# Performance work log

Hardware: AMD Instinct MI355X
Metric: run time of the kernel (lower is better)

## Reference

```python
import jax, jax.numpy as jnp
import numpy as np

# (in_ch, out_ch) per conv layer per SA stage (use_xyz adds +3 to first in-ch)
DIMS = {1: [(3, 64), (64, 64), (64, 128)],
        2: [(131, 128), (128, 128), (128, 256)],
        3: [(259, 256), (256, 512), (512, 1024)]}
B, N = 32, 4096


def setup_inputs() -> dict:
    key = jax.random.key(0)
    key, k = jax.random.split(key)
    inp = {"pointcloud": jax.random.uniform(k, (B, N, 3), jnp.float32)}
    for s in (1, 2, 3):
        for l, (ci, co) in enumerate(DIMS[s]):
            key, k1, k2, k3 = jax.random.split(key, 4)
            inp[f"w{s}{l}"] = jax.random.normal(k1, (ci, co), jnp.float32) * (1.0 / np.sqrt(ci))
            # eval-mode BatchNorm folded to per-channel scale g and bias b
            inp[f"g{s}{l}"] = 1.0 + 0.1 * jax.random.normal(k2, (co,), jnp.float32)
            inp[f"b{s}{l}"] = 0.1 * jax.random.normal(k3, (co,), jnp.float32)
    return inp


def fps(xyz, npoint):
    """Farthest point sampling. xyz: (B,N,3) -> idx (B,npoint) int32. First index is 0."""
    n = xyz.shape[1]
    def one(pts):
        def body(carry, _):
            dist, last = carry
            d = jnp.sum((pts - pts[last]) ** 2, axis=-1)
            dist = jnp.minimum(dist, d)
            nxt = jnp.argmax(dist).astype(jnp.int32)
            return (dist, nxt), nxt
        init = (jnp.full((n,), 1e10, pts.dtype), jnp.int32(0))
        _, idxs = jax.lax.scan(body, init, None, length=npoint - 1)
        return jnp.concatenate([jnp.zeros((1,), jnp.int32), idxs])
    return jax.vmap(one)(xyz)


def ball_query(xyz, centers, radius, nsample):
    """xyz (B,N,3), centers (B,S,3) -> idx (B,S,nsample): first nsample in-ball point
    indices, deficits padded with the first found index (matches CUDA ball_query)."""
    n = xyz.shape[1]
    d2 = jnp.sum((centers[:, :, None, :] - xyz[:, None, :, :]) ** 2, axis=-1)  # (B,S,N)
    keyv = jnp.where(d2 < radius * radius, jnp.arange(n)[None, None, :], n)
    sk = jnp.sort(keyv, axis=-1)[..., :nsample]  # ascending valid indices, pad = n
    first = sk[..., :1]
    idx = jnp.where(sk == n, first, sk)
    return jnp.clip(idx, 0, n - 1)


def gather(pts, idx):
    """pts (B,N,C), idx (B,...) -> (B,...,C)"""
    return jax.vmap(lambda p, i: p[i])(pts, idx)


def shared_mlp(x, params):
    """x (..., Cin); each layer: 1x1 conv (matmul) + folded-BN affine + ReLU."""
    for w, g, b in params:
        x = jax.nn.relu(jnp.einsum('...c,cd->...d', x, w) * g + b)
    return x


def sa_module(xyz, feat, npoint, radius, nsample, params):
    ctr_idx = fps(xyz, npoint)
    new_xyz = gather(xyz, ctr_idx)                        # (B,S,3)
    idx = ball_query(xyz, new_xyz, radius, nsample)       # (B,S,K)
    g_xyz = gather(xyz, idx) - new_xyz[:, :, None, :]     # (B,S,K,3) centered
    grouped = g_xyz if feat is None else jnp.concatenate([g_xyz, gather(feat, idx)], axis=-1)
    h = shared_mlp(grouped, params)                       # (B,S,K,Cout)
    return new_xyz, jnp.max(h, axis=2)                    # max-pool over neighbors


def reference(pointcloud, w10, g10, b10, w11, g11, b11, w12, g12, b12,
              w20, g20, b20, w21, g21, b21, w22, g22, b22,
              w30, g30, b30, w31, g31, b31, w32, g32, b32):
    p1 = [(w10, g10, b10), (w11, g11, b11), (w12, g12, b12)]
    p2 = [(w20, g20, b20), (w21, g21, b21), (w22, g22, b22)]
    p3 = [(w30, g30, b30), (w31, g31, b31), (w32, g32, b32)]
    xyz = pointcloud[..., :3]
    xyz, feat = sa_module(xyz, None, 512, 0.2, 64, p1)
    xyz, feat = sa_module(xyz, feat, 128, 0.4, 64, p2)
    # group-all SA: one group containing all points, xyz NOT centered
    grouped = jnp.concatenate([xyz, feat], axis=-1)[:, None]  # (B,1,S,259)
    h = shared_mlp(grouped, p3)                                # (B,1,S,1024)
    return jnp.max(h, axis=2)[:, 0]                            # (B,1024)
```

## Files before the change

### kernel.cpp

```cpp
#include <hip/hip_runtime.h>
#include <math.h>

#define NTH 256

using short8 = __attribute__((ext_vector_type(8))) short;
using f32x4  = __attribute__((ext_vector_type(4))) float;

__device__ __forceinline__ unsigned short f2bf(float x) {
    unsigned u = __float_as_uint(x);
    u += 0x7fff + ((u >> 16) & 1);
    return (unsigned short)(u >> 16);
}
__device__ __forceinline__ float bf2f(unsigned short h) {
    return __uint_as_float(((unsigned)h) << 16);
}

template<int CTRL>
__device__ __forceinline__ unsigned long long dppmax(unsigned long long k) {
    unsigned lo = (unsigned)k, hi = (unsigned)(k >> 32);
    unsigned plo = (unsigned)__builtin_amdgcn_update_dpp(0, (int)lo, CTRL, 0xF, 0xF, true);
    unsigned phi = (unsigned)__builtin_amdgcn_update_dpp(0, (int)hi, CTRL, 0xF, 0xF, true);
    unsigned long long p = ((unsigned long long)phi << 32) | plo;
    return p > k ? p : k;
}

template<int N, int NPOINT, int NTHR>
__device__ __forceinline__ void fps_body(
    const float* __restrict__ xyz, float* __restrict__ out_xyz, int b,
    float* __restrict__ pts , float* __restrict__ ctr ,
    unsigned long long* __restrict__ wkey )
{
    constexpr int PT = N / NTHR;
    constexpr int NW = NTHR / 64;
    const int tid  = threadIdx.x;
    const int lane = tid & 63;
    const int w    = tid >> 6;
    const float* src = xyz + (size_t)b * N * 3;

    for (int e = tid; e < N * 3; e += NTHR) pts[e] = src[e];

    float px[PT], py[PT], pz[PT], dist[PT];
    unsigned klo[PT];
#pragma unroll
    for (int j = 0; j < PT; ++j) {
        int i = j * NTHR + tid;
        px[j] = src[i * 3 + 0]; py[j] = src[i * 3 + 1]; pz[j] = src[i * 3 + 2];
        dist[j] = 1e10f;
        klo[j] = ~(unsigned)i;
    }
    if (tid == 0) { ctr[0] = src[0]; ctr[1] = src[1]; ctr[2] = src[2]; }
    __syncthreads();

    int last = 0;
    for (int it = 1; it < NPOINT; ++it) {
        const float lx = pts[last * 3 + 0];
        const float ly = pts[last * 3 + 1];
        const float lz = pts[last * 3 + 2];
        unsigned long long best = 0ull;
#pragma unroll
        for (int j = 0; j < PT; ++j) {
            float dx = px[j] - lx, dy = py[j] - ly, dz = pz[j] - lz;
            float d = __fadd_rn(__fadd_rn(__fmul_rn(dx, dx), __fmul_rn(dy, dy)),
                                __fmul_rn(dz, dz));
            float nd = fminf(dist[j], d);
            dist[j] = nd;
            unsigned long long key =
                ((unsigned long long)__float_as_uint(nd) << 32) | (unsigned long long)klo[j];
            best = (key > best) ? key : best;
        }
        best = dppmax<0xB1>(best);
        best = dppmax<0x4E>(best);
        best = dppmax<0x141>(best);
        best = dppmax<0x140>(best);
        best = dppmax<0x142>(best);
        best = dppmax<0x143>(best);
        const int p = (it & 1) * NW;
        if (lane == 63) wkey[p + w] = best;
        __syncthreads();
        unsigned long long K0[NW];
#pragma unroll
        for (int v = 0; v < NW; ++v) K0[v] = wkey[p + v];
#pragma unroll
        for (int st = NW / 2; st > 0; st >>= 1)
#pragma unroll
            for (int v = 0; v < st; ++v) K0[v] = (K0[v + st] > K0[v]) ? K0[v + st] : K0[v];
        last = (int)(~(unsigned)K0[0]);
        if (tid == 0) {
            ctr[it * 3 + 0] = pts[last * 3 + 0];
            ctr[it * 3 + 1] = pts[last * 3 + 1];
            ctr[it * 3 + 2] = pts[last * 3 + 2];
        }
    }
    __syncthreads();
    float* dst = out_xyz + (size_t)b * NPOINT * 3;
    for (int e = tid; e < NPOINT * 3; e += NTHR) dst[e] = ctr[e];
}

#define PREP_TOT 813056
__device__ __forceinline__ void prep_body(
    int gid, int stride,
    const float* __restrict__ w0, const float* __restrict__ w1, const float* __restrict__ w2,
    const float* __restrict__ w3, const float* __restrict__ w4, const float* __restrict__ w5,
    const float* __restrict__ w6, const float* __restrict__ w7, const float* __restrict__ w8,
    unsigned short* __restrict__ outw)
{
    const int K_[9]    = {3, 64, 64, 131, 128, 128, 259, 256, 512};
    const int N_[9]    = {64, 64, 128, 128, 128, 256, 256, 512, 1024};
    const int E_[9]    = {2048, 4096, 8192, 20480, 16384, 32768, 73728, 131072, 524288};
    const int base_[9] = {0, 4096, 12288, 28672, 69632, 102400, 167936, 315392, 577536};
    const int PCF_[9]  = {0, 0, 0, 128, 0, 0, 256, 0, 0};
    const float* W_[9] = {w0, w1, w2, w3, w4, w5, w6, w7, w8};
    for (; gid < PREP_TOT; gid += stride) {
        int i = 0, t = gid;
        while (t >= E_[i]) { t -= E_[i]; ++i; }
        const int Nn = N_[i];
        const int k8 = t / (Nn * 8);
        const int rem = t - k8 * Nn * 8;
        const int col = rem >> 3, j = rem & 7;
        const int k = k8 * 8 + j;
        float v = 0.f;
        if (k < K_[i]) {
            int ks = k;
            const int pcf = PCF_[i];
            if (pcf > 0) ks = (k < pcf) ? (k + 3) : (k - pcf);
            v = W_[i][(size_t)ks * Nn + col];
        }
        unsigned short hi = f2bf(v);
        unsigned short lo = f2bf(v - bf2f(hi));
        outw[base_[i] + t] = hi;
        outw[base_[i] + E_[i] + t] = lo;
    }
}

template<int N1, int NP1>
__global__ __launch_bounds__(NTH) void fps1_prep(
    const float* __restrict__ pc, float* __restrict__ nxyz1,
    const float* __restrict__ w0, const float* __restrict__ w1, const float* __restrict__ w2,
    const float* __restrict__ w3, const float* __restrict__ w4, const float* __restrict__ w5,
    const float* __restrict__ w6, const float* __restrict__ w7, const float* __restrict__ w8,
    unsigned short* __restrict__ outw, int nfps)
{
    __shared__ float pts[N1 * 3];
    __shared__ float ctr[NP1 * 3];
    __shared__ unsigned long long fwk[2 * (NTH / 64)];
    if ((int)blockIdx.x < nfps) {
        fps_body<N1, NP1, NTH>(pc, nxyz1, blockIdx.x, pts, ctr, fwk);
    } else {
        prep_body((blockIdx.x - nfps) * NTH + threadIdx.x,
                  (gridDim.x - nfps) * NTH,
                  w0, w1, w2, w3, w4, w5, w6, w7, w8, outw);
    }
}

__global__ __launch_bounds__(NTH) void ball_query_kernel(
    const float* __restrict__ xyz, const float* __restrict__ centers,
    int* __restrict__ out, int BS, int N, int S, float r2)
{
    const int wid = blockIdx.x * (NTH / 64) + (threadIdx.x >> 6);
    if (wid >= BS) return;
    const int lane = threadIdx.x & 63;
    const int b = wid / S;
    const float cx = centers[(size_t)wid * 3 + 0];
    const float cy = centers[(size_t)wid * 3 + 1];
    const float cz = centers[(size_t)wid * 3 + 2];
    const float* px = xyz + (size_t)b * N * 3;
    int count = 0, first = -1;
    for (int base = 0; base < N && count < 64; base += 64) {
        int i = base + lane;
        float dx = px[i * 3 + 0] - cx, dy = px[i * 3 + 1] - cy, dz = px[i * 3 + 2] - cz;
        float d2 = __fadd_rn(__fadd_rn(__fmul_rn(dx, dx), __fmul_rn(dy, dy)),
                             __fmul_rn(dz, dz));
        bool inb = d2 < r2;
        unsigned long long m = __ballot(inb);
        if (first < 0 && m) first = base + (__ffsll(m) - 1);
        if (inb) {
            int pos = count + (int)__popcll(m & ((1ull << lane) - 1ull));
            if (pos < 64) out[(size_t)wid * 64 + pos] = i;
        }
        count += (int)__popcll(m);
    }
    int cnt = count > 64 ? 64 : count;
    if (first < 0) first = N - 1;
    if (lane >= cnt) out[(size_t)wid * 64 + lane] = first;
}

template<int K, int NSUB, int NOFF, int NFULL, int RTILES, int SX, int SY, bool FINAL>
__device__ __forceinline__ void mfma_layer(
    const unsigned short* __restrict__ whi, const unsigned short* __restrict__ wlo,
    const float* __restrict__ gm, const float* __restrict__ bt,
    const unsigned short* __restrict__ Xhi, const unsigned short* __restrict__ Xlo,
    unsigned short* __restrict__ Yhi, unsigned short* __restrict__ Ylo,
    float* outp, int tid)
{
    constexpr int KP  = (K + 31) & ~31;
    constexpr int KC  = KP / 32;
    constexpr int NTW = NSUB / 64;
    static_assert(NSUB % 64 == 0, "col split");
    const int w = tid >> 6, lane = tid & 63;
    const int lr = lane & 15, lg = lane >> 4;
    const int colbase = NOFF + w * (NSUB / 4);

    f32x4 acc[RTILES][NTW];
#pragma unroll
    for (int m = 0; m < RTILES; ++m)
#pragma unroll
        for (int t = 0; t < NTW; ++t) acc[m][t] = f32x4{0.f, 0.f, 0.f, 0.f};

    const unsigned short* xh0 = Xhi + lr * SX + lg * 8;
    const unsigned short* xl0 = Xlo + lr * SX + lg * 8;

    for (int kc = 0; kc < KC; ++kc) {
        const size_t krow = (size_t)(kc * 4 + lg) * NFULL * 8;
        short8 bh[NTW], bl[NTW];
#pragma unroll
        for (int t = 0; t < NTW; ++t) {
            const int col = colbase + t * 16 + lr;
            bh[t] = *reinterpret_cast<const short8*>(whi + krow + (size_t)col * 8);
            bl[t] = *reinterpret_cast<const short8*>(wlo + krow + (size_t)col * 8);
        }
#pragma unroll
        for (int m = 0; m < RTILES; ++m) {
            short8 ah = *reinterpret_cast<const short8*>(xh0 + m * 16 * SX + kc * 32);
            short8 al = *reinterpret_cast<const short8*>(xl0 + m * 16 * SX + kc * 32);
#pragma unroll
            for (int t = 0; t < NTW; ++t) {
                acc[m][t] = __builtin_amdgcn_mfma_f32_16x16x32_bf16(ah, bh[t], acc[m][t], 0, 0, 0);
                acc[m][t] = __builtin_amdgcn_mfma_f32_16x16x32_bf16(ah, bl[t], acc[m][t], 0, 0, 0);
                acc[m][t] = __builtin_amdgcn_mfma_f32_16x16x32_bf16(al, bh[t], acc[m][t], 0, 0, 0);
            }
        }
    }
#pragma unroll
    for (int t = 0; t < NTW; ++t) {
        const int col = colbase + t * 16 + lr;
        const float gv = gm[col], bv = bt[col];
        if constexpr (FINAL) {
            float mx = 0.f;
#pragma unroll
            for (int m = 0; m < RTILES; ++m)
#pragma unroll
                for (int r = 0; r < 4; ++r)
                    mx = fmaxf(mx, fmaxf(fmaf(acc[m][t][r], gv, bv), 0.f));
            mx = fmaxf(mx, __shfl_xor(mx, 16));
            mx = fmaxf(mx, __shfl_xor(mx, 32));
            if (lg == 0)
                atomicMax(reinterpret_cast<int*>(outp) + col, __float_as_int(mx));
        } else {
#pragma unroll
            for (int m = 0; m < RTILES; ++m)
#pragma unroll
                for (int r = 0; r < 4; ++r) {
                    float v = fmaxf(fmaf(acc[m][t][r], gv, bv), 0.f);
                    unsigned short hi = f2bf(v);
                    unsigned short lo = f2bf(v - bf2f(hi));
                    const int row = m * 16 + lg * 4 + r;
                    Yhi[row * SY + col] = hi;
                    Ylo[row * SY + col] = lo;
                }
        }
    }
}

template<int CF, int C0, int C1, int C2, int R>
struct SaCfg {
    static constexpr int CIN = 3 + CF;
    static constexpr int KP0 = (CIN + 31) & ~31;
    static constexpr int SX = KP0 + 8, SY1 = C0 + 8, SY2 = C1 + 8;
    static constexpr int RT = R / 16;
    static constexpr int HALVES = 64 / R;
    static constexpr int OFF_Y1 = 0;
    static constexpr int OFF_X = 2 * R * SY1;
    static constexpr int XSZ = 2 * R * SX, Y2SZ = 2 * R * SY2;
    static constexpr int TOT = OFF_X + (XSZ > Y2SZ ? XSZ : Y2SZ);
};

template<int CF, int C0, int C1, int C2, int R>
__device__ __forceinline__ void sa_body(
    unsigned short* __restrict__ sm, int flat,
    const float* __restrict__ src_xyz, const float* __restrict__ src_feat,
    const float* __restrict__ centers, const int* __restrict__ nbr,
    const unsigned short* __restrict__ w0h, const unsigned short* __restrict__ w0l,
    const unsigned short* __restrict__ w1h, const unsigned short* __restrict__ w1l,
    const unsigned short* __restrict__ w2h, const unsigned short* __restrict__ w2l,
    const float* __restrict__ g0, const float* __restrict__ b0,
    const float* __restrict__ g1, const float* __restrict__ b1,
    const float* __restrict__ g2, const float* __restrict__ b2,
    float* __restrict__ out_feat, int S, int N)
{
    using C = SaCfg<CF, C0, C1, C2, R>;
    constexpr int TPR = NTH / R;
    const int tid  = threadIdx.x;
    const int half = flat % C::HALVES;
    const int bs   = flat / C::HALVES;
    const int b    = bs / S;
    const int* __restrict__ myidx = nbr + (size_t)bs * 64 + half * R;

    unsigned short* Xhi = sm + C::OFF_X;    unsigned short* Xlo = Xhi + R * C::SX;
    unsigned short* Y1h = sm + C::OFF_Y1;   unsigned short* Y1l = Y1h + R * C::SY1;
    unsigned short* Y2h = sm + C::OFF_X;    unsigned short* Y2l = Y2h + R * C::SY2;

    const float cx = centers[(size_t)bs * 3 + 0];
    const float cy = centers[(size_t)bs * 3 + 1];
    const float cz = centers[(size_t)bs * 3 + 2];

    {
        const int r = tid / TPR, s = tid % TPR;
        const int pid = myidx[r];
        unsigned short* xh = Xhi + r * C::SX;
        unsigned short* xl = Xlo + r * C::SX;
        if constexpr (CF > 0) {
            constexpr int CPT = CF / TPR;
            const float* frow = src_feat + ((size_t)b * N + pid) * CF + s * CPT;
#pragma unroll
            for (int q = 0; q < CPT / 4; ++q) {
                float4 v4 = *reinterpret_cast<const float4*>(frow + q * 4);
                ushort4 h, l;
                h.x = f2bf(v4.x); l.x = f2bf(v4.x - bf2f(h.x));
                h.y = f2bf(v4.y); l.y = f2bf(v4.y - bf2f(h.y));
                h.z = f2bf(v4.z); l.z = f2bf(v4.z - bf2f(h.z));
                h.w = f2bf(v4.w); l.w = f2bf(v4.w - bf2f(h.w));
                *reinterpret_cast<ushort4*>(xh + s * CPT + q * 4) = h;
                *reinterpret_cast<ushort4*>(xl + s * CPT + q * 4) = l;
            }
        }
        if (s < 3) {
            float p = src_xyz[((size_t)b * N + pid) * 3 + s]
                      - (s == 0 ? cx : (s == 1 ? cy : cz));
            unsigned short hi = f2bf(p), lo = f2bf(p - bf2f(hi));
            xh[CF + s] = hi; xl[CF + s] = lo;
        }
        constexpr int PADPER = (C::KP0 - C::CIN + TPR - 1) / TPR;
#pragma unroll
        for (int q = 0; q < PADPER; ++q) {
            int c = C::CIN + s * PADPER + q;
            if (c < C::KP0) { xh[c] = 0; xl[c] = 0; }
        }
    }
    __syncthreads();
    mfma_layer<C::CIN, C0, 0, C0, C::RT, C::SX, C::SY1, false>(
        w0h, w0l, g0, b0, Xhi, Xlo, Y1h, Y1l, nullptr, tid);
    __syncthreads();
    mfma_layer<C0, C1, 0, C1, C::RT, C::SY1, C::SY2, false>(
        w1h, w1l, g1, b1, Y1h, Y1l, Y2h, Y2l, nullptr, tid);
    __syncthreads();
    mfma_layer<C1, C2, 0, C2, C::RT, C::SY2, 0, true>(
        w2h, w2l, g2, b2, Y2h, Y2l, nullptr, nullptr,
        out_feat + (size_t)bs * C2, tid);
}

template<int CF, int C0, int C1, int C2, int R>
__global__ __launch_bounds__(NTH) void sa_mfma(
    const float* __restrict__ src_xyz, const float* __restrict__ src_feat,
    const float* __restrict__ centers, const int* __restrict__ nbr,
    const unsigned short* __restrict__ w0h, const unsigned short* __restrict__ w0l,
    const unsigned short* __restrict__ w1h, const unsigned short* __restrict__ w1l,
    const unsigned short* __restrict__ w2h, const unsigned short* __restrict__ w2l,
    const float* __restrict__ g0, const float* __restrict__ b0,
    const float* __restrict__ g1, const float* __restrict__ b1,
    const float* __restrict__ g2, const float* __restrict__ b2,
    float* __restrict__ out_feat, int S, int N)
{
    __shared__ __align__(16) unsigned short sm[SaCfg<CF, C0, C1, C2, R>::TOT];
    sa_body<CF, C0, C1, C2, R>(sm, blockIdx.x, src_xyz, src_feat, centers, nbr,
                               w0h, w0l, w1h, w1l, w2h, w2l,
                               g0, b0, g1, b1, g2, b2, out_feat, S, N);
}

template<int CF, int C0, int C1, int C2, int R, int N2, int NP2>
__global__ __launch_bounds__(NTH) void sa1_fps2(
    const float* __restrict__ src_xyz, const float* __restrict__ src_feat,
    const float* __restrict__ centers, const int* __restrict__ nbr,
    const unsigned short* __restrict__ w0h, const unsigned short* __restrict__ w0l,
    const unsigned short* __restrict__ w1h, const unsigned short* __restrict__ w1l,
    const unsigned short* __restrict__ w2h, const unsigned short* __restrict__ w2l,
    const float* __restrict__ g0, const float* __restrict__ b0,
    const float* __restrict__ g1, const float* __restrict__ b1,
    const float* __restrict__ g2, const float* __restrict__ b2,
    float* __restrict__ out_feat, int S, int N,
    const float* __restrict__ fps_in, float* __restrict__ fps_out, int NSA)
{
    __shared__ __align__(16) unsigned short sm[SaCfg<CF, C0, C1, C2, R>::TOT];
    __shared__ float fpts[N2 * 3];
    __shared__ float fctr[NP2 * 3];
    __shared__ unsigned long long fwk[2 * (NTH / 64)];
    if ((int)blockIdx.x < NSA) {
        sa_body<CF, C0, C1, C2, R>(sm, blockIdx.x,
                                   src_xyz, src_feat, centers, nbr,
                                   w0h, w0l, w1h, w1l, w2h, w2l,
                                   g0, b0, g1, b1, g2, b2, out_feat, S, N);
    } else {
        fps_body<N2, NP2, NTH>(fps_in, fps_out, blockIdx.x - NSA, fpts, fctr, fwk);
    }
}

template<int CF, int C0, int C1, int C2>
__global__ __launch_bounds__(NTH) void head_mfma(
    const float* __restrict__ xyz, const float* __restrict__ feat,
    const unsigned short* __restrict__ w0h, const unsigned short* __restrict__ w0l,
    const unsigned short* __restrict__ w1h, const unsigned short* __restrict__ w1l,
    const unsigned short* __restrict__ w2h, const unsigned short* __restrict__ w2l,
    const float* __restrict__ g0, const float* __restrict__ b0,
    const float* __restrict__ g1, const float* __restrict__ b1,
    const float* __restrict__ g2, const float* __restrict__ b2,
    float* __restrict__ out, int Np)
{
    constexpr int R = 16;
    constexpr int CIN = 3 + CF;
    constexpr int KP0 = (CIN + 31) & ~31;
    constexpr int SX = KP0 + 8, SY1 = C0 + 8, SY2 = C1 + 8;
    constexpr int OFF_Y1 = 0;
    constexpr int OFF_X  = 2 * R * SY1;
    constexpr int XSZ = 2 * R * SX, Y2SZ = 2 * R * SY2;
    constexpr int TOT = OFF_X + (XSZ > Y2SZ ? XSZ : Y2SZ);
    __shared__ __align__(16) unsigned short sm[TOT];
    constexpr int TPR = NTH / R;

    const int tid = threadIdx.x;
    const int chunks = Np / R;
    const int b  = blockIdx.x / chunks;
    const int r0 = (blockIdx.x % chunks) * R;

    unsigned short* Xhi = sm + OFF_X;   unsigned short* Xlo = Xhi + R * SX;
    unsigned short* Y1h = sm + OFF_Y1;  unsigned short* Y1l = Y1h + R * SY1;
    unsigned short* Y2h = sm + OFF_X;   unsigned short* Y2l = Y2h + R * SY2;

    {
        const int r = tid / TPR, s = tid % TPR;
        const int row = r0 + r;
        unsigned short* xh = Xhi + r * SX;
        unsigned short* xl = Xlo + r * SX;
        constexpr int CPT = CF / TPR;
        const float* frow = feat + ((size_t)b * Np + row) * CF + s * CPT;
#pragma unroll
        for (int q = 0; q < CPT / 4; ++q) {
            float4 v4 = *reinterpret_cast<const float4*>(frow + q * 4);
            ushort4 h, l;
            h.x = f2bf(v4.x); l.x = f2bf(v4.x - bf2f(h.x));
            h.y = f2bf(v4.y); l.y = f2bf(v4.y - bf2f(h.y));
            h.z = f2bf(v4.z); l.z = f2bf(v4.z - bf2f(h.z));
            h.w = f2bf(v4.w); l.w = f2bf(v4.w - bf2f(h.w));
            *reinterpret_cast<ushort4*>(xh + s * CPT + q * 4) = h;
            *reinterpret_cast<ushort4*>(xl + s * CPT + q * 4) = l;
        }
        if (s < 3) {
            float p = xyz[((size_t)b * Np + row) * 3 + s];
            unsigned short hi = f2bf(p), lo = f2bf(p - bf2f(hi));
            xh[CF + s] = hi; xl[CF + s] = lo;
        }
        constexpr int PADPER = (KP0 - CIN + TPR - 1) / TPR;
#pragma unroll
        for (int q = 0; q < PADPER; ++q) {
            int c = CIN + s * PADPER + q;
            if (c < KP0) { xh[c] = 0; xl[c] = 0; }
        }
    }
    __syncthreads();
    mfma_layer<CIN, C0, 0, C0, 1, SX, SY1, false>(w0h, w0l, g0, b0, Xhi, Xlo, Y1h, Y1l, nullptr, tid);
    __syncthreads();
    mfma_layer<C0, C1, 0, C1, 1, SY1, SY2, false>(w1h, w1l, g1, b1, Y1h, Y1l, Y2h, Y2l, nullptr, tid);
    __syncthreads();
    float* op = out + (size_t)b * C2;
    mfma_layer<C1, C2 / 2, 0,      C2, 1, SY2, 0, true>(w2h, w2l, g2, b2, Y2h, Y2l, nullptr, nullptr, op, tid);
    mfma_layer<C1, C2 / 2, C2 / 2, C2, 1, SY2, 0, true>(w2h, w2l, g2, b2, Y2h, Y2l, nullptr, nullptr, op, tid);
}

extern "C" void kernel_launch(void* const* d_in, const int* in_sizes, int n_in,
                              void* d_out, int out_size, void* d_ws, size_t ws_size,
                              hipStream_t stream)
{
    (void)in_sizes; (void)n_in; (void)ws_size;
    const int B = 32, N = 4096;
    const float* pc = (const float*)d_in[0];
    const float* W[27];
    for (int i = 0; i < 27; ++i) W[i] = (const float*)d_in[1 + i];
    float* out = (float*)d_out;

    char* ws = (char*)d_ws;
    size_t off = 0;
    auto take = [&](size_t bytes) {
        void* p = ws + off;
        off += (bytes + 255) & ~(size_t)255;
        return p;
    };
    float* nxyz1 = (float*)take((size_t)B * 512 * 3 * 4);
    int*   idx1  = (int*)  take((size_t)B * 512 * 64 * 4);
    float* feat1 = (float*)take((size_t)B * 512 * 128 * 4);
    float* nxyz2 = (float*)take((size_t)B * 128 * 3 * 4);
    int*   idx2  = (int*)  take((size_t)B * 128 * 64 * 4);
    float* feat2 = (float*)take((size_t)B * 128 * 256 * 4);
    unsigned short* wf = (unsigned short*)take((size_t)1626112 * 2);

    const int E_[9]    = {2048, 4096, 8192, 20480, 16384, 32768, 73728, 131072, 524288};
    const int base_[9] = {0, 4096, 12288, 28672, 69632, 102400, 167936, 315392, 577536};
    const unsigned short* wh[9]; const unsigned short* wl[9];
    for (int i = 0; i < 9; ++i) { wh[i] = wf + base_[i]; wl[i] = wf + base_[i] + E_[i]; }

    hipMemsetAsync(feat1, 0, (size_t)B * 512 * 128 * 4, stream);
    hipMemsetAsync(feat2, 0, (size_t)B * 128 * 256 * 4, stream);
    hipMemsetAsync(d_out, 0, (size_t)out_size * 4, stream);

    fps1_prep<4096, 512><<<32 + 512, NTH, 0, stream>>>(
        pc, nxyz1,
        W[0], W[3], W[6], W[9], W[12], W[15], W[18], W[21], W[24],
        wf, 32);

    ball_query_kernel<<<(B * 512 + 3) / 4, NTH, 0, stream>>>(
        pc, nxyz1, idx1, B * 512, N, 512, (float)(0.2 * 0.2));
    sa1_fps2<0, 64, 64, 128, 64, 512, 128><<<B * 512 + B, NTH, 0, stream>>>(
        pc, nullptr, nxyz1, idx1,
        wh[0], wl[0], wh[1], wl[1], wh[2], wl[2],
        W[1], W[2], W[4], W[5], W[7], W[8],
        feat1, 512, N,
        nxyz1, nxyz2, B * 512);

    ball_query_kernel<<<(B * 128 + 3) / 4, NTH, 0, stream>>>(
        nxyz1, nxyz2, idx2, B * 128, 512, 128, (float)(0.4 * 0.4));
    sa_mfma<128, 128, 128, 256, 32><<<B * 128 * 2, NTH, 0, stream>>>(
        nxyz1, feat1, nxyz2, idx2,
        wh[3], wl[3], wh[4], wl[4], wh[5], wl[5],
        W[10], W[11], W[13], W[14], W[16], W[17],
        feat2, 128, 512);

    head_mfma<256, 256, 512, 1024><<<B * 8, NTH, 0, stream>>>(
        nxyz2, feat2,
        wh[6], wl[6], wh[7], wl[7], wh[8], wl[8],
        W[19], W[20], W[22], W[23], W[25], W[26],
        out, 128);
}
```

Before: 721.2 us.

## Split FPS into halves overlapped with SA1 and fuse ball query into SA

FPS for stage 1 is split into two chunks of 256 centroids, with the distance state spilled to global memory between launches. The SA1 MLP for the first 256 centroids then runs in the same launch as the second FPS half, and the second SA1 half runs alongside stage-2 FPS. The standalone ball_query kernels are removed. Each SA block now does its own ball query with 4 waves scanning quarter segments and merging the results in LDS. FPS waves get raised scheduling priority so the serial FPS chain is not starved by co-resident MLP blocks. The costs are an extra launch, the dist spill traffic, and ball-query work repeated in both halves of SA2.

```diff
diff --git a/kernel.cpp b/kernel.cpp
--- a/kernel.cpp
+++ b/kernel.cpp
@@ -24,11 +24,12 @@
     return p > k ? p : k;
 }
 
-template<int N, int NPOINT, int NTHR>
+template<int N, int NPOINT, int NTHR, int NPC, bool INIT, bool SPILL>
 __device__ __forceinline__ void fps_body(
-    const float* __restrict__ xyz, float* __restrict__ out_xyz, int b,
+    const float* __restrict__ xyz, float* __restrict__ out_xyz, int b, int it0,
     float* __restrict__ pts , float* __restrict__ ctr ,
-    unsigned long long* __restrict__ wkey )
+    unsigned long long* __restrict__ wkey ,
+    float* __restrict__ sdist, int* __restrict__ slast)
 {
     constexpr int PT = N / NTHR;
     constexpr int NW = NTHR / 64;
@@ -37,6 +38,8 @@
     const int w    = tid >> 6;
     const float* src = xyz + (size_t)b * N * 3;
 
+    __builtin_amdgcn_s_setprio(1);
+
     for (int e = tid; e < N * 3; e += NTHR) pts[e] = src[e];
 
     float px[PT], py[PT], pz[PT], dist[PT];
@@ -45,14 +48,22 @@
     for (int j = 0; j < PT; ++j) {
         int i = j * NTHR + tid;
         px[j] = src[i * 3 + 0]; py[j] = src[i * 3 + 1]; pz[j] = src[i * 3 + 2];
+        klo[j] = ~(unsigned)i;
         dist[j] = 1e10f;
-        klo[j] = ~(unsigned)i;
-    }
-    if (tid == 0) { ctr[0] = src[0]; ctr[1] = src[1]; ctr[2] = src[2]; }
-    __syncthreads();
-
+    }
     int last = 0;
-    for (int it = 1; it < NPOINT; ++it) {
+    if constexpr (!INIT) {
+        const float* sd = sdist + (size_t)b * N;
+#pragma unroll
+        for (int j = 0; j < PT; ++j) dist[j] = sd[j * NTHR + tid];
+        last = slast[b];
+    } else {
+        if (tid == 0) { ctr[0] = src[0]; ctr[1] = src[1]; ctr[2] = src[2]; }
+    }
+    __syncthreads();
+
+    constexpr int CBEG = INIT ? 1 : 0;
+    for (int c = CBEG; c < NPC; ++c) {
         const float lx = pts[last * 3 + 0];
         const float ly = pts[last * 3 + 1];
         const float lz = pts[last * 3 + 2];
@@ -74,7 +85,7 @@
         best = dppmax<0x140>(best);
         best = dppmax<0x142>(best);
         best = dppmax<0x143>(best);
-        const int p = (it & 1) * NW;
+        const int p = (c & 1) * NW;
         if (lane == 63) wkey[p + w] = best;
         __syncthreads();
         unsigned long long K0[NW];
@@ -86,14 +97,21 @@
             for (int v = 0; v < st; ++v) K0[v] = (K0[v + st] > K0[v]) ? K0[v + st] : K0[v];
         last = (int)(~(unsigned)K0[0]);
         if (tid == 0) {
-            ctr[it * 3 + 0] = pts[last * 3 + 0];
-            ctr[it * 3 + 1] = pts[last * 3 + 1];
-            ctr[it * 3 + 2] = pts[last * 3 + 2];
-        }
-    }
-    __syncthreads();
-    float* dst = out_xyz + (size_t)b * NPOINT * 3;
-    for (int e = tid; e < NPOINT * 3; e += NTHR) dst[e] = ctr[e];
+            ctr[c * 3 + 0] = pts[last * 3 + 0];
+            ctr[c * 3 + 1] = pts[last * 3 + 1];
+            ctr[c * 3 + 2] = pts[last * 3 + 2];
+        }
+    }
+    __syncthreads();
+    if constexpr (SPILL) {
+        float* sd = sdist + (size_t)b * N;
+#pragma unroll
+        for (int j = 0; j < PT; ++j) sd[j * NTHR + tid] = dist[j];
+        if (tid == 0) slast[b] = last;
+    }
+    float* dst = out_xyz + ((size_t)b * NPOINT + (it0 - CBEG)) * 3;
+    for (int e = tid; e < NPC * 3; e += NTHR) dst[e] = ctr[e];
+    __builtin_amdgcn_s_setprio(0);
 }
 
 #define PREP_TOT 813056
@@ -132,58 +150,6 @@
     }
 }
 
-template<int N1, int NP1>
-__global__ __launch_bounds__(NTH) void fps1_prep(
-    const float* __restrict__ pc, float* __restrict__ nxyz1,
-    const float* __restrict__ w0, const float* __restrict__ w1, const float* __restrict__ w2,
-    const float* __restrict__ w3, const float* __restrict__ w4, const float* __restrict__ w5,
-    const float* __restrict__ w6, const float* __restrict__ w7, const float* __restrict__ w8,
-    unsigned short* __restrict__ outw, int nfps)
-{
-    __shared__ float pts[N1 * 3];
-    __shared__ float ctr[NP1 * 3];
-    __shared__ unsigned long long fwk[2 * (NTH / 64)];
-    if ((int)blockIdx.x < nfps) {
-        fps_body<N1, NP1, NTH>(pc, nxyz1, blockIdx.x, pts, ctr, fwk);
-    } else {
-        prep_body((blockIdx.x - nfps) * NTH + threadIdx.x,
-                  (gridDim.x - nfps) * NTH,
-                  w0, w1, w2, w3, w4, w5, w6, w7, w8, outw);
-    }
-}
-
-__global__ __launch_bounds__(NTH) void ball_query_kernel(
-    const float* __restrict__ xyz, const float* __restrict__ centers,
-    int* __restrict__ out, int BS, int N, int S, float r2)
-{
-    const int wid = blockIdx.x * (NTH / 64) + (threadIdx.x >> 6);
-    if (wid >= BS) return;
-    const int lane = threadIdx.x & 63;
-    const int b = wid / S;
-    const float cx = centers[(size_t)wid * 3 + 0];
-    const float cy = centers[(size_t)wid * 3 + 1];
-    const float cz = centers[(size_t)wid * 3 + 2];
-    const float* px = xyz + (size_t)b * N * 3;
-    int count = 0, first = -1;
-    for (int base = 0; base < N && count < 64; base += 64) {
-        int i = base + lane;
-        float dx = px[i * 3 + 0] - cx, dy = px[i * 3 + 1] - cy, dz = px[i * 3 + 2] - cz;
-        float d2 = __fadd_rn(__fadd_rn(__fmul_rn(dx, dx), __fmul_rn(dy, dy)),
-                             __fmul_rn(dz, dz));
-        bool inb = d2 < r2;
-        unsigned long long m = __ballot(inb);
-        if (first < 0 && m) first = base + (__ffsll(m) - 1);
-        if (inb) {
-            int pos = count + (int)__popcll(m & ((1ull << lane) - 1ull));
-            if (pos < 64) out[(size_t)wid * 64 + pos] = i;
-        }
-        count += (int)__popcll(m);
-    }
-    int cnt = count > 64 ? 64 : count;
-    if (first < 0) first = N - 1;
-    if (lane >= cnt) out[(size_t)wid * 64 + lane] = first;
-}
-
 template<int K, int NSUB, int NOFF, int NFULL, int RTILES, int SX, int SY, bool FINAL>
 __device__ __forceinline__ void mfma_layer(
     const unsigned short* __restrict__ whi, const unsigned short* __restrict__ wlo,
@@ -267,45 +233,86 @@
     static constexpr int KP0 = (CIN + 31) & ~31;
     static constexpr int SX = KP0 + 8, SY1 = C0 + 8, SY2 = C1 + 8;
     static constexpr int RT = R / 16;
-    static constexpr int HALVES = 64 / R;
     static constexpr int OFF_Y1 = 0;
     static constexpr int OFF_X = 2 * R * SY1;
     static constexpr int XSZ = 2 * R * SX, Y2SZ = 2 * R * SY2;
     static constexpr int TOT = OFF_X + (XSZ > Y2SZ ? XSZ : Y2SZ);
+    static constexpr int BYTES = TOT * 2 + 264 * 4;
 };
 
 template<int CF, int C0, int C1, int C2, int R>
 __device__ __forceinline__ void sa_body(
-    unsigned short* __restrict__ sm, int flat,
+    unsigned short* __restrict__ sm, int* __restrict__ bqm,
+    int b, int cs, int S, int half,
     const float* __restrict__ src_xyz, const float* __restrict__ src_feat,
-    const float* __restrict__ centers, const int* __restrict__ nbr,
+    const float* __restrict__ centers,
     const unsigned short* __restrict__ w0h, const unsigned short* __restrict__ w0l,
     const unsigned short* __restrict__ w1h, const unsigned short* __restrict__ w1l,
     const unsigned short* __restrict__ w2h, const unsigned short* __restrict__ w2l,
     const float* __restrict__ g0, const float* __restrict__ b0,
     const float* __restrict__ g1, const float* __restrict__ b1,
     const float* __restrict__ g2, const float* __restrict__ b2,
-    float* __restrict__ out_feat, int S, int N)
+    float* __restrict__ out_feat, int N, float r2)
 {
     using C = SaCfg<CF, C0, C1, C2, R>;
     constexpr int TPR = NTH / R;
     const int tid  = threadIdx.x;
-    const int half = flat % C::HALVES;
-    const int bs   = flat / C::HALVES;
-    const int b    = bs / S;
-    const int* __restrict__ myidx = nbr + (size_t)bs * 64 + half * R;
+    const int lane = tid & 63;
+    const int w    = tid >> 6;
+    const int bs   = b * S + cs;
+
+    const float cx = centers[(size_t)bs * 3 + 0];
+    const float cy = centers[(size_t)bs * 3 + 1];
+    const float cz = centers[(size_t)bs * 3 + 2];
+
+    {
+        const int seg = N >> 2;
+        const float* px = src_xyz + (size_t)b * N * 3;
+        int count = 0, first = -1;
+        const int bend = (w + 1) * seg;
+        for (int base = w * seg; base < bend && count < 64; base += 64) {
+            int i = base + lane;
+            float dx = px[i * 3 + 0] - cx, dy = px[i * 3 + 1] - cy, dz = px[i * 3 + 2] - cz;
+            float d2 = __fadd_rn(__fadd_rn(__fmul_rn(dx, dx), __fmul_rn(dy, dy)),
+                                 __fmul_rn(dz, dz));
+            bool inb = d2 < r2;
+            unsigned long long m = __ballot(inb);
+            if (first < 0 && m) first = base + (__ffsll(m) - 1);
+            if (inb) {
+                int pos = count + (int)__popcll(m & ((1ull << lane) - 1ull));
+                if (pos < 64) bqm[w * 64 + pos] = i;
+            }
+            count += (int)__popcll(m);
+        }
+        if (lane == 0) {
+            bqm[256 + w] = count > 64 ? 64 : count;
+            bqm[260 + w] = first;
+        }
+    }
+    __syncthreads();
 
     unsigned short* Xhi = sm + C::OFF_X;    unsigned short* Xlo = Xhi + R * C::SX;
     unsigned short* Y1h = sm + C::OFF_Y1;   unsigned short* Y1l = Y1h + R * C::SY1;
     unsigned short* Y2h = sm + C::OFF_X;    unsigned short* Y2l = Y2h + R * C::SY2;
 
-    const float cx = centers[(size_t)bs * 3 + 0];
-    const float cy = centers[(size_t)bs * 3 + 1];
-    const float cz = centers[(size_t)bs * 3 + 2];
-
     {
         const int r = tid / TPR, s = tid % TPR;
-        const int pid = myidx[r];
+        int pid;
+        {
+            const int cA = bqm[256 + 0], cB = bqm[256 + 1], cC = bqm[256 + 2], cD = bqm[256 + 3];
+            const int tot = cA + cB + cC + cD;
+            int t = half * R + r;
+            if (t < tot) {
+                int ww = 0;
+                if (t >= cA) { t -= cA; ww = 1;
+                    if (t >= cB) { t -= cB; ww = 2;
+                        if (t >= cC) { t -= cC; ww = 3; } } }
+                pid = bqm[ww * 64 + t];
+            } else {
+                const int fA = bqm[260 + 0], fB = bqm[260 + 1], fC = bqm[260 + 2], fD = bqm[260 + 3];
+                pid = fA >= 0 ? fA : (fB >= 0 ? fB : (fC >= 0 ? fC : (fD >= 0 ? fD : (N - 1))));
+            }
+        }
         unsigned short* xh = Xhi + r * C::SX;
         unsigned short* xl = Xlo + r * C::SX;
         if constexpr (CF > 0) {
@@ -348,49 +355,116 @@
         out_feat + (size_t)bs * C2, tid);
 }
 
-template<int CF, int C0, int C1, int C2, int R>
-__global__ __launch_bounds__(NTH) void sa_mfma(
-    const float* __restrict__ src_xyz, const float* __restrict__ src_feat,
-    const float* __restrict__ centers, const int* __restrict__ nbr,
+template<int N1>
+__global__ __launch_bounds__(NTH) void k_fps1a_prep(
+    const float* __restrict__ pc, float* __restrict__ nxyz1,
+    const float* __restrict__ w0, const float* __restrict__ w1, const float* __restrict__ w2,
+    const float* __restrict__ w3, const float* __restrict__ w4, const float* __restrict__ w5,
+    const float* __restrict__ w6, const float* __restrict__ w7, const float* __restrict__ w8,
+    unsigned short* __restrict__ outw,
+    float* __restrict__ sdist, int* __restrict__ slast, int nfps)
+{
+    __shared__ float pts[N1 * 3];
+    __shared__ float ctr[256 * 3];
+    __shared__ unsigned long long wkey[2 * (NTH / 64)];
+    if ((int)blockIdx.x < nfps) {
+        fps_body<N1, 512, NTH, 256, true, true>(pc, nxyz1, blockIdx.x, 1,
+                                                pts, ctr, wkey, sdist, slast);
+    } else {
+        prep_body((blockIdx.x - nfps) * NTH + threadIdx.x,
+                  (gridDim.x - nfps) * NTH,
+                  w0, w1, w2, w3, w4, w5, w6, w7, w8, outw);
+    }
+}
+
+__global__ __launch_bounds__(NTH) void k_fps1b_sa1h1(
+    const float* __restrict__ pc, float* __restrict__ nxyz1,
+    float* __restrict__ sdist, int* __restrict__ slast,
     const unsigned short* __restrict__ w0h, const unsigned short* __restrict__ w0l,
     const unsigned short* __restrict__ w1h, const unsigned short* __restrict__ w1l,
     const unsigned short* __restrict__ w2h, const unsigned short* __restrict__ w2l,
     const float* __restrict__ g0, const float* __restrict__ b0,
     const float* __restrict__ g1, const float* __restrict__ b1,
     const float* __restrict__ g2, const float* __restrict__ b2,
-    float* __restrict__ out_feat, int S, int N)
-{
-    __shared__ __align__(16) unsigned short sm[SaCfg<CF, C0, C1, C2, R>::TOT];
-    sa_body<CF, C0, C1, C2, R>(sm, blockIdx.x, src_xyz, src_feat, centers, nbr,
-                               w0h, w0l, w1h, w1l, w2h, w2l,
-                               g0, b0, g1, b1, g2, b2, out_feat, S, N);
-}
-
-template<int CF, int C0, int C1, int C2, int R, int N2, int NP2>
-__global__ __launch_bounds__(NTH) void sa1_fps2(
-    const float* __restrict__ src_xyz, const float* __restrict__ src_feat,
-    const float* __restrict__ centers, const int* __restrict__ nbr,
+    float* __restrict__ feat1, float r2)
+{
+    constexpr int FPSB = 4096 * 3 * 4 + 256 * 3 * 4 + 2 * (NTH / 64) * 8;
+    constexpr int SAB  = SaCfg<0, 64, 64, 128, 64>::BYTES;
+    constexpr int BYTES = FPSB > SAB ? FPSB : SAB;
+    __shared__ __align__(16) char raw[BYTES];
+    if ((int)blockIdx.x < 32) {
+        float* pts = (float*)raw;
+        float* ctr = (float*)(raw + 4096 * 3 * 4);
+        unsigned long long* wkey = (unsigned long long*)(raw + 4096 * 3 * 4 + 256 * 3 * 4);
+        fps_body<4096, 512, NTH, 256, false, false>(pc, nxyz1, blockIdx.x, 256,
+                                                    pts, ctr, wkey, sdist, slast);
+    } else {
+        const int blk = blockIdx.x - 32;
+        const int b = blk >> 8, cs = blk & 255;
+        unsigned short* sm = (unsigned short*)raw;
+        int* bqm = (int*)(raw + SaCfg<0, 64, 64, 128, 64>::TOT * 2);
+        sa_body<0, 64, 64, 128, 64>(sm, bqm, b, cs, 512, 0,
+                                    pc, nullptr, nxyz1,
+                                    w0h, w0l, w1h, w1l, w2h, w2l,
+                                    g0, b0, g1, b1, g2, b2, feat1, 4096, r2);
+    }
+}
+
+__global__ __launch_bounds__(NTH) void k_fps2_sa1h2(
+    const float* __restrict__ pc, const float* __restrict__ nxyz1_c,
+    float* __restrict__ nxyz1, float* __restrict__ nxyz2,
     const unsigned short* __restrict__ w0h, const unsigned short* __restrict__ w0l,
     const unsigned short* __restrict__ w1h, const unsigned short* __restrict__ w1l,
     const unsigned short* __restrict__ w2h, const unsigned short* __restrict__ w2l,
     const float* __restrict__ g0, const float* __restrict__ b0,
     const float* __restrict__ g1, const float* __restrict__ b1,
     const float* __restrict__ g2, const float* __restrict__ b2,
-    float* __restrict__ out_feat, int S, int N,
-    const float* __restrict__ fps_in, float* __restrict__ fps_out, int NSA)
-{
-    __shared__ __align__(16) unsigned short sm[SaCfg<CF, C0, C1, C2, R>::TOT];
-    __shared__ float fpts[N2 * 3];
-    __shared__ float fctr[NP2 * 3];
-    __shared__ unsigned long long fwk[2 * (NTH / 64)];
-    if ((int)blockIdx.x < NSA) {
-        sa_body<CF, C0, C1, C2, R>(sm, blockIdx.x,
-                                   src_xyz, src_feat, centers, nbr,
-                                   w0h, w0l, w1h, w1l, w2h, w2l,
-                                   g0, b0, g1, b1, g2, b2, out_feat, S, N);
+    float* __restrict__ feat1, float r2)
+{
+    constexpr int FPSB = 512 * 3 * 4 + 128 * 3 * 4 + 2 * (NTH / 64) * 8;
+    constexpr int SAB  = SaCfg<0, 64, 64, 128, 64>::BYTES;
+    constexpr int BYTES = FPSB > SAB ? FPSB : SAB;
+    __shared__ __align__(16) char raw[BYTES];
+    if ((int)blockIdx.x < 32) {
+        float* pts = (float*)raw;
+        float* ctr = (float*)(raw + 512 * 3 * 4);
+        unsigned long long* wkey = (unsigned long long*)(raw + 512 * 3 * 4 + 128 * 3 * 4);
+        fps_body<512, 128, NTH, 128, true, false>(nxyz1, nxyz2, blockIdx.x, 1,
+                                                  pts, ctr, wkey, nullptr, nullptr);
     } else {
-        fps_body<N2, NP2, NTH>(fps_in, fps_out, blockIdx.x - NSA, fpts, fctr, fwk);
-    }
+        const int blk = blockIdx.x - 32;
+        const int b = blk >> 8, cs = 256 + (blk & 255);
+        unsigned short* sm = (unsigned short*)raw;
+        int* bqm = (int*)(raw + SaCfg<0, 64, 64, 128, 64>::TOT * 2);
+        sa_body<0, 64, 64, 128, 64>(sm, bqm, b, cs, 512, 0,
+                                    pc, nullptr, nxyz1_c,
+                                    w0h, w0l, w1h, w1l, w2h, w2l,
+                                    g0, b0, g1, b1, g2, b2, feat1, 4096, r2);
+    }
+}
+
+__global__ __launch_bounds__(NTH) void k_sa2(
+    const float* __restrict__ nxyz1, const float* __restrict__ feat1,
+    const float* __restrict__ nxyz2,
+    const unsigned short* __restrict__ w0h, const unsigned short* __restrict__ w0l,
+    const unsigned short* __restrict__ w1h, const unsigned short* __restrict__ w1l,
+    const unsigned short* __restrict__ w2h, const unsigned short* __restrict__ w2l,
+    const float* __restrict__ g0, const float* __restrict__ b0,
+    const float* __restrict__ g1, const float* __restrict__ b1,
+    const float* __restrict__ g2, const float* __restrict__ b2,
+    float* __restrict__ feat2, float r2)
+{
+    using C = SaCfg<128, 128, 128, 256, 32>;
+    __shared__ __align__(16) char raw[C::BYTES];
+    const int half = blockIdx.x & 1;
+    const int cb   = blockIdx.x >> 1;
+    const int b = cb >> 7, cs = cb & 127;
+    unsigned short* sm = (unsigned short*)raw;
+    int* bqm = (int*)(raw + C::TOT * 2);
+    sa_body<128, 128, 128, 256, 32>(sm, bqm, b, cs, 128, half,
+                                    nxyz1, feat1, nxyz2,
+                                    w0h, w0l, w1h, w1l, w2h, w2l,
+                                    g0, b0, g1, b1, g2, b2, feat2, 512, r2);
 }
 
 template<int CF, int C0, int C1, int C2>
@@ -469,7 +543,7 @@
                               hipStream_t stream)
 {
     (void)in_sizes; (void)n_in; (void)ws_size;
-    const int B = 32, N = 4096;
+    const int B = 32;
     const float* pc = (const float*)d_in[0];
     const float* W[27];
     for (int i = 0; i < 27; ++i) W[i] = (const float*)d_in[1 + i];
@@ -483,12 +557,12 @@
         return p;
     };
     float* nxyz1 = (float*)take((size_t)B * 512 * 3 * 4);
-    int*   idx1  = (int*)  take((size_t)B * 512 * 64 * 4);
     float* feat1 = (float*)take((size_t)B * 512 * 128 * 4);
     float* nxyz2 = (float*)take((size_t)B * 128 * 3 * 4);
-    int*   idx2  = (int*)  take((size_t)B * 128 * 64 * 4);
     float* feat2 = (float*)take((size_t)B * 128 * 256 * 4);
     unsigned short* wf = (unsigned short*)take((size_t)1626112 * 2);
+    float* sdist = (float*)take((size_t)B * 4096 * 4);
+    int*   slast = (int*)take((size_t)B * 4);
 
     const int E_[9]    = {2048, 4096, 8192, 20480, 16384, 32768, 73728, 131072, 524288};
     const int base_[9] = {0, 4096, 12288, 28672, 69632, 102400, 167936, 315392, 577536};
@@ -499,27 +573,31 @@
     hipMemsetAsync(feat2, 0, (size_t)B * 128 * 256 * 4, stream);
     hipMemsetAsync(d_out, 0, (size_t)out_size * 4, stream);
 
-    fps1_prep<4096, 512><<<32 + 512, NTH, 0, stream>>>(
+    const float r2_1 = (float)(0.2 * 0.2);
+    const float r2_2 = (float)(0.4 * 0.4);
+
+    k_fps1a_prep<4096><<<32 + 512, NTH, 0, stream>>>(
         pc, nxyz1,
         W[0], W[3], W[6], W[9], W[12], W[15], W[18], W[21], W[24],
-        wf, 32);
-
-    ball_query_kernel<<<(B * 512 + 3) / 4, NTH, 0, stream>>>(
-        pc, nxyz1, idx1, B * 512, N, 512, (float)(0.2 * 0.2));
-    sa1_fps2<0, 64, 64, 128, 64, 512, 128><<<B * 512 + B, NTH, 0, stream>>>(
-        pc, nullptr, nxyz1, idx1,
+        wf, sdist, slast, 32);
+
+    k_fps1b_sa1h1<<<32 + B * 256, NTH, 0, stream>>>(
+        pc, nxyz1, sdist, slast,
         wh[0], wl[0], wh[1], wl[1], wh[2], wl[2],
         W[1], W[2], W[4], W[5], W[7], W[8],
-        feat1, 512, N,
-        nxyz1, nxyz2, B * 512);
-
-    ball_query_kernel<<<(B * 128 + 3) / 4, NTH, 0, stream>>>(
-        nxyz1, nxyz2, idx2, B * 128, 512, 128, (float)(0.4 * 0.4));
-    sa_mfma<128, 128, 128, 256, 32><<<B * 128 * 2, NTH, 0, stream>>>(
-        nxyz1, feat1, nxyz2, idx2,
+        feat1, r2_1);
+
+    k_fps2_sa1h2<<<32 + B * 256, NTH, 0, stream>>>(
+        pc, nxyz1, nxyz1, nxyz2,
+        wh[0], wl[0], wh[1], wl[1], wh[2], wl[2],
+        W[1], W[2], W[4], W[5], W[7], W[8],
+        feat1, r2_1);
+
+    k_sa2<<<B * 128 * 2, NTH, 0, stream>>>(
+        nxyz1, feat1, nxyz2,
         wh[3], wl[3], wh[4], wl[4], wh[5], wl[5],
         W[10], W[11], W[13], W[14], W[16], W[17],
-        feat2, 128, 512);
+        feat2, r2_2);
 
     head_mfma<256, 256, 512, 1024><<<B * 8, NTH, 0, stream>>>(
         nxyz2, feat2,
```

Result: faster. 612.4 us (-15.1%).
